# Optimization experiments

Measured on AMD Instinct MI355X. Metric: run time of the kernel, lower is better.

The kernel has to match this reference:

```python
import jax, jax.numpy as jnp
import numpy as np

B, S, DD, DE, DA = 32, 2048, 1024, 1024, 1024
NEG = -1000000000.0


def setup_inputs() -> dict:
    key = jax.random.key(0)
    k1, k2, k3, k4, k5 = jax.random.split(key, 5)
    query_state = jax.random.normal(k1, (B, DD), dtype=jnp.float32)
    encoder_hidden_states = jax.random.normal(k2, (B, S, DE), dtype=jnp.float32)
    attention_mask = jax.random.randint(k3, (B, S), 0, 2, dtype=jnp.int32)
    # W_c: Linear(DD+DE -> DA, bias=False): weight shape [DA, DD+DE]
    W_c = jax.random.normal(k4, (DA, DD + DE), dtype=jnp.float32) / np.sqrt(DD + DE)
    # V: Linear(DA -> 1, bias=False): weight shape [1, DA]
    V = jax.random.normal(k5, (1, DA), dtype=jnp.float32) / np.sqrt(DA)
    return {
        "query_state": query_state,
        "encoder_hidden_states": encoder_hidden_states,
        "attention_mask": attention_mask,
        "W_c": W_c,
        "V": V,
    }


def reference(query_state, encoder_hidden_states, attention_mask, W_c, V):
    # Split W_c along input dim: cat([q, e]) @ W_c.T == q @ Wq.T + e @ We.T
    Wq = W_c[:, :DD]          # [DA, DD]
    We = W_c[:, DD:]          # [DA, DE]
    q_proj = jnp.einsum('bd,ad->ba', query_state, Wq)            # [B, DA]
    e_proj = jnp.einsum('bsd,ad->bsa', encoder_hidden_states, We)  # [B, S, DA]
    energies = jnp.tanh(q_proj[:, None, :] + e_proj)             # [B, S, DA]
    scores = jnp.einsum('bsa,a->bs', energies, V[0])             # [B, S]
    scores = jnp.where(attention_mask == 0, NEG, scores)
    attention_weights = jax.nn.softmax(scores, axis=1)           # [B, S]
    context_vector = jnp.einsum('bs,bsd->bd', attention_weights, encoder_hidden_states)
    return context_vector, attention_weights
```

## Files before the change

kernel.cpp:

```cpp
#include <hip/hip_runtime.h>
#include <hip/hip_bf16.h>

#define NB 32
#define NS 2048
#define NDD 1024
#define NDE 1024
#define NDA 1024
#define NEGV (-1000000000.0f)

typedef __attribute__((ext_vector_type(8))) __bf16 bf16x8;
typedef __attribute__((ext_vector_type(4))) float f32x4;

__device__ __forceinline__ float fast_tanh(float x) {
    x = fminf(10.0f, fmaxf(-10.0f, x));
    float e = __expf(2.0f * x);
    return __fdividef(e - 1.0f, e + 1.0f);
}

__device__ __forceinline__ float bfu2f(unsigned short v) {
    union { unsigned u; float f; } c; c.u = (unsigned)v << 16; return c.f;
}

__global__ void prep_we(const float* __restrict__ Wc, __bf16* __restrict__ We) {
    int f = blockIdx.x * 256 + threadIdx.x;
    int a  = f >> 8;
    int k4 = f & 255;
    float4 v = *reinterpret_cast<const float4*>(Wc + (size_t)a * (NDD + NDE) + NDD + k4 * 4);
    union { __bf16 h[4]; uint2 u; } pk;
    pk.h[0] = (__bf16)v.x; pk.h[1] = (__bf16)v.y;
    pk.h[2] = (__bf16)v.z; pk.h[3] = (__bf16)v.w;
    *reinterpret_cast<uint2*>(We + (size_t)a * NDE + k4 * 4) = pk.u;
}

__global__ void prep_e(const float* __restrict__ E, __bf16* __restrict__ Eb) {
    size_t i = ((size_t)blockIdx.x * 256 + threadIdx.x) * 8;
    f32x4 x = __builtin_nontemporal_load(reinterpret_cast<const f32x4*>(E + i));
    f32x4 y = __builtin_nontemporal_load(reinterpret_cast<const f32x4*>(E + i + 4));
    union { __bf16 h[8]; uint4 u; } pk;
    pk.h[0] = (__bf16)x[0]; pk.h[1] = (__bf16)x[1]; pk.h[2] = (__bf16)x[2]; pk.h[3] = (__bf16)x[3];
    pk.h[4] = (__bf16)y[0]; pk.h[5] = (__bf16)y[1]; pk.h[6] = (__bf16)y[2]; pk.h[7] = (__bf16)y[3];
    *reinterpret_cast<uint4*>(Eb + i) = pk.u;
}

__global__ void qproj_kernel(const float* __restrict__ q, const float* __restrict__ Wc,
                             float* __restrict__ qp) {
    __shared__ float qs[NDD];
    int b = blockIdx.y;
    int a = blockIdx.x * 256 + threadIdx.x;
    float4 qv = *reinterpret_cast<const float4*>(q + (size_t)b * NDD + threadIdx.x * 4);
    *reinterpret_cast<float4*>(qs + threadIdx.x * 4) = qv;
    __syncthreads();
    const float* wrow = Wc + (size_t)a * (NDD + NDE);
    float acc = 0.f;
#pragma unroll 4
    for (int k4 = 0; k4 < 256; ++k4) {
        float4 w = *reinterpret_cast<const float4*>(wrow + k4 * 4);
        acc += qs[k4*4+0] * w.x + qs[k4*4+1] * w.y + qs[k4*4+2] * w.z + qs[k4*4+3] * w.w;
    }
    qp[(size_t)b * NDA + a] = acc;
}

__global__ __launch_bounds__(512, 2) void score256(
    const __bf16* __restrict__ Eb, const __bf16* __restrict__ We,
    const float* __restrict__ qp, const float* __restrict__ Vv,
    float* __restrict__ sp) {
    __shared__ __align__(16) __bf16 As[2][256 * 64];
    __shared__ __align__(16) __bf16 Bs[2][256 * 64];

    const int tid  = threadIdx.x;
    const int lane = tid & 63;
    const int l15  = lane & 15;
    const int h    = lane >> 4;
    const int wid  = tid >> 6;
    const int wr   = wid >> 2;
    const int wc   = wid & 3;

    const int bid = blockIdx.x;
    const int xcd = bid & 7;
    const int j   = bid >> 3;
    const int m   = xcd * 32 + (j >> 2);
    const int n   = j & 3;
    const int row0  = m * 256;
    const int ncol0 = n * 256;
    const int b     = m >> 3;

    f32x4 acc[8][4];
#pragma unroll
    for (int mf = 0; mf < 8; ++mf)
#pragma unroll
        for (int nf = 0; nf < 4; ++nf)
            acc[mf][nf] = (f32x4){0.f, 0.f, 0.f, 0.f};

    int offE[4], offW[4];
#pragma unroll
    for (int i = 0; i < 4; ++i) {
        int rr = i * 64 + (tid >> 3);
        int sg = (tid & 7) ^ (rr & 7);
        offE[i] = (row0  + rr) * 1024 + sg * 8;
        offW[i] = (ncol0 + rr) * 1024 + sg * 8;
    }

    const int slot0 = ((h ^ (l15 & 7)) * 16);
    const int aoffl = (wr * 128 + l15) * 128 + slot0;
    const int boffl = (wc * 64  + l15) * 128 + slot0;

#define STAGE8(abuf, bbuf, kc)                                                          \
    {                                                                                   \
        _Pragma("unroll")                                                               \
        for (int i = 0; i < 4; ++i)                                                     \
            __builtin_amdgcn_global_load_lds(                                           \
                (const __attribute__((address_space(1))) unsigned*)(Eb + offE[i] + (kc)),\
                (__attribute__((address_space(3))) unsigned*)((char*)(abuf) + i * 8192 + wid * 1024), \
                16, 0, 0);                                                              \
        _Pragma("unroll")                                                               \
        for (int i = 0; i < 4; ++i)                                                     \
            __builtin_amdgcn_global_load_lds(                                           \
                (const __attribute__((address_space(1))) unsigned*)(We + offW[i] + (kc)),\
                (__attribute__((address_space(3))) unsigned*)((char*)(bbuf) + i * 8192 + wid * 1024), \
                16, 0, 0);                                                              \
    }

    STAGE8(&As[0][0], &Bs[0][0], 0)
    float qv[4], vv[4];
#pragma unroll
    for (int nf = 0; nf < 4; ++nf) {
        int col = ncol0 + wc * 64 + nf * 16 + l15;
        qv[nf] = qp[(size_t)b * NDA + col];
        vv[nf] = Vv[col];
    }
    __syncthreads();

    for (int T = 0; T < 16; ++T) {
        const int cur = T & 1;
        const char* Ab = (const char*)&As[cur][0];
        const char* Bb = (const char*)&Bs[cur][0];
        if (T < 15) STAGE8(&As[cur ^ 1][0], &Bs[cur ^ 1][0], (T + 1) * 64)

        bf16x8 bfr[4][2], afr[4][2];
#pragma unroll
        for (int nf = 0; nf < 4; ++nf) {
            bfr[nf][0] = *reinterpret_cast<const bf16x8*>(Bb + (boffl + nf * 2048));
            bfr[nf][1] = *reinterpret_cast<const bf16x8*>(Bb + ((boffl + nf * 2048) ^ 64));
        }
#pragma unroll
        for (int mi = 0; mi < 4; ++mi) {
            afr[mi][0] = *reinterpret_cast<const bf16x8*>(Ab + (aoffl + mi * 2048));
            afr[mi][1] = *reinterpret_cast<const bf16x8*>(Ab + ((aoffl + mi * 2048) ^ 64));
        }
        __builtin_amdgcn_s_setprio(1);
#pragma unroll
        for (int ks = 0; ks < 2; ++ks)
#pragma unroll
            for (int mi = 0; mi < 4; ++mi)
#pragma unroll
                for (int nf = 0; nf < 4; ++nf)
                    acc[mi][nf] = __builtin_amdgcn_mfma_f32_16x16x32_bf16(afr[mi][ks], bfr[nf][ks], acc[mi][nf], 0, 0, 0);
        __builtin_amdgcn_s_setprio(0);
#pragma unroll
        for (int mi = 0; mi < 4; ++mi) {
            afr[mi][0] = *reinterpret_cast<const bf16x8*>(Ab + (aoffl + (4 + mi) * 2048));
            afr[mi][1] = *reinterpret_cast<const bf16x8*>(Ab + ((aoffl + (4 + mi) * 2048) ^ 64));
        }
        __builtin_amdgcn_s_setprio(1);
#pragma unroll
        for (int ks = 0; ks < 2; ++ks)
#pragma unroll
            for (int mi = 0; mi < 4; ++mi)
#pragma unroll
                for (int nf = 0; nf < 4; ++nf)
                    acc[4 + mi][nf] = __builtin_amdgcn_mfma_f32_16x16x32_bf16(afr[mi][ks], bfr[nf][ks], acc[4 + mi][nf], 0, 0, 0);
        __builtin_amdgcn_s_setprio(0);
        __syncthreads();
    }

    float* ps2 = reinterpret_cast<float*>(&As[0][0]);
#pragma unroll
    for (int mf = 0; mf < 8; ++mf)
#pragma unroll
        for (int jj = 0; jj < 4; ++jj) {
            float s = 0.f;
#pragma unroll
            for (int nf = 0; nf < 4; ++nf)
                s += fast_tanh(qv[nf] + acc[mf][nf][jj]) * vv[nf];
            s += __shfl_xor(s, 1);
            s += __shfl_xor(s, 2);
            s += __shfl_xor(s, 4);
            s += __shfl_xor(s, 8);
            if (l15 == 0)
                ps2[(wr * 128 + mf * 16 + h * 4 + jj) * 4 + wc] = s;
        }
    __syncthreads();
    if (tid < 256)
        sp[(size_t)n * (NB * NS) + row0 + tid] =
            ps2[tid * 4] + ps2[tid * 4 + 1] + ps2[tid * 4 + 2] + ps2[tid * 4 + 3];
}

__global__ void softmax_kernel(const float* __restrict__ sp, const int* __restrict__ mask,
                               float* __restrict__ wout, int np) {
    int b = blockIdx.x;
    const int* mrow = mask + (size_t)b * NS;
    float v[8];
    float lmax = -INFINITY;
#pragma unroll
    for (int jj = 0; jj < 8; ++jj) {
        int s = threadIdx.x + 256 * jj;
        float sc = 0.f;
        for (int nn = 0; nn < np; ++nn) sc += sp[(size_t)nn * (NB * NS) + b * NS + s];
        v[jj] = (mrow[s] == 0) ? NEGV : sc;
        lmax = fmaxf(lmax, v[jj]);
    }
#pragma unroll
    for (int mm = 1; mm <= 32; mm <<= 1) lmax = fmaxf(lmax, __shfl_xor(lmax, mm));
    __shared__ float redm[4], reds[4];
    if ((threadIdx.x & 63) == 0) redm[threadIdx.x >> 6] = lmax;
    __syncthreads();
    float bmax = fmaxf(fmaxf(redm[0], redm[1]), fmaxf(redm[2], redm[3]));
    float lsum = 0.f;
#pragma unroll
    for (int jj = 0; jj < 8; ++jj) { v[jj] = __expf(v[jj] - bmax); lsum += v[jj]; }
#pragma unroll
    for (int mm = 1; mm <= 32; mm <<= 1) lsum += __shfl_xor(lsum, mm);
    if ((threadIdx.x & 63) == 0) reds[threadIdx.x >> 6] = lsum;
    __syncthreads();
    float inv = __fdividef(1.0f, reds[0] + reds[1] + reds[2] + reds[3]);
#pragma unroll
    for (int jj = 0; jj < 8; ++jj) wout[(size_t)b * NS + threadIdx.x + 256 * jj] = v[jj] * inv;
}

__global__ void context_bf16(const __bf16* __restrict__ Eb, const float* __restrict__ w,
                             float* __restrict__ ctx) {
    int b  = blockIdx.x >> 3;
    int dc = blockIdx.x & 7;
    int dg = threadIdx.x & 31;
    int ss = threadIdx.x >> 5;
    const __bf16* base = Eb + (size_t)b * NS * NDE + (size_t)(ss * 256) * NDE + dc * 128 + dg * 4;
    const float* wb = w + (size_t)b * NS + ss * 256;
    float a0 = 0.f, a1 = 0.f, a2 = 0.f, a3 = 0.f;
#pragma unroll 8
    for (int s = 0; s < 256; ++s) {
        float ws = wb[s];
        uint2 u = *reinterpret_cast<const uint2*>(base + (size_t)s * NDE);
        a0 = fmaf(ws, bfu2f((unsigned short)(u.x & 0xffff)), a0);
        a1 = fmaf(ws, bfu2f((unsigned short)(u.x >> 16)), a1);
        a2 = fmaf(ws, bfu2f((unsigned short)(u.y & 0xffff)), a2);
        a3 = fmaf(ws, bfu2f((unsigned short)(u.y >> 16)), a3);
    }
    __shared__ float4 part[256];
    part[threadIdx.x] = make_float4(a0, a1, a2, a3);
    __syncthreads();
    if (threadIdx.x < 32) {
        float4 r = part[threadIdx.x];
#pragma unroll
        for (int k = 1; k < 8; ++k) {
            float4 p = part[threadIdx.x + 32 * k];
            r.x += p.x; r.y += p.y; r.z += p.z; r.w += p.w;
        }
        *reinterpret_cast<float4*>(ctx + (size_t)b * NDD + dc * 128 + threadIdx.x * 4) = r;
    }
}

extern "C" void kernel_launch(void* const* d_in, const int* in_sizes, int n_in,
                              void* d_out, int out_size, void* d_ws, size_t ws_size,
                              hipStream_t stream) {
    const float* query = (const float*)d_in[0];
    const float* enc   = (const float*)d_in[1];
    const int*   mask  = (const int*)d_in[2];
    const float* Wc    = (const float*)d_in[3];
    const float* V     = (const float*)d_in[4];

    float* out = (float*)d_out;
    float* ctx = out;
    float* wts = out + NB * NDD;

    const size_t WE_B = (size_t)NDA * NDE * 2;
    const size_t QP_B = (size_t)NB * NDA * 4;
    const size_t SP_B = (size_t)8 * NB * NS * 4;
    char* ws = (char*)d_ws;
    __bf16* We = (__bf16*)ws;
    float*  qp = (float*)(ws + WE_B);
    float*  sp = (float*)(ws + WE_B + QP_B);
    __bf16* Eb = (__bf16*)(ws + WE_B + QP_B + SP_B);

    hipLaunchKernelGGL(prep_we,      dim3(1024),  dim3(256), 0, stream, Wc, We);
    hipLaunchKernelGGL(qproj_kernel, dim3(4, NB), dim3(256), 0, stream, query, Wc, qp);
    hipLaunchKernelGGL(prep_e,       dim3(32768), dim3(256), 0, stream, enc, Eb);
    hipLaunchKernelGGL(score256,     dim3(1024),  dim3(512), 0, stream, Eb, We, qp, V, sp);
    hipLaunchKernelGGL(softmax_kernel, dim3(NB),  dim3(256), 0, stream, sp, mask, wts, 4);
    hipLaunchKernelGGL(context_bf16, dim3(256),   dim3(256), 0, stream, Eb, wts, ctx);
}
```

Before: 295.4 us.

## Split score GEMM tile across 16 waves with 1024-thread blocks

Doubles the score GEMM block from 512 to 1024 threads (16 waves in a 4x4 grid). Each wave now owns a 64x64 sub-tile instead of 128x64, halving per-wave accumulators and per-thread async loads per stage. The K loop is restructured to load and multiply one k-slice at a time. The aim is more waves to hide latency and lower register pressure. In exchange, occupancy falls to one block per CU, and each barrier now synchronizes more waves.

```diff
diff --git a/kernel.cpp b/kernel.cpp
--- a/kernel.cpp
+++ b/kernel.cpp
@@ -60,7 +60,7 @@
     qp[(size_t)b * NDA + a] = acc;
 }
 
-__global__ __launch_bounds__(512, 2) void score256(
+__global__ __launch_bounds__(1024, 1) void score256(
     const __bf16* __restrict__ Eb, const __bf16* __restrict__ We,
     const float* __restrict__ qp, const float* __restrict__ Vv,
     float* __restrict__ sp) {
@@ -84,43 +84,44 @@
     const int ncol0 = n * 256;
     const int b     = m >> 3;
 
-    f32x4 acc[8][4];
-#pragma unroll
-    for (int mf = 0; mf < 8; ++mf)
+    f32x4 acc[4][4];
+#pragma unroll
+    for (int mf = 0; mf < 4; ++mf)
 #pragma unroll
         for (int nf = 0; nf < 4; ++nf)
             acc[mf][nf] = (f32x4){0.f, 0.f, 0.f, 0.f};
 
-    int offE[4], offW[4];
-#pragma unroll
-    for (int i = 0; i < 4; ++i) {
-        int rr = i * 64 + (tid >> 3);
-        int sg = (tid & 7) ^ (rr & 7);
-        offE[i] = (row0  + rr) * 1024 + sg * 8;
-        offW[i] = (ncol0 + rr) * 1024 + sg * 8;
+    int offE[2], offW[2];
+#pragma unroll
+    for (int i = 0; i < 2; ++i) {
+        int chunk = i * 1024 + tid;
+        int r  = chunk >> 3;
+        int sg = (chunk & 7) ^ (r & 7);
+        offE[i] = (row0  + r) * 1024 + sg * 8;
+        offW[i] = (ncol0 + r) * 1024 + sg * 8;
     }
 
     const int slot0 = ((h ^ (l15 & 7)) * 16);
-    const int aoffl = (wr * 128 + l15) * 128 + slot0;
-    const int boffl = (wc * 64  + l15) * 128 + slot0;
-
-#define STAGE8(abuf, bbuf, kc)                                                          \
+    const int aoffl = (wr * 64 + l15) * 128 + slot0;
+    const int boffl = (wc * 64 + l15) * 128 + slot0;
+
+#define STAGE4(abuf, bbuf, kc)                                                          \
     {                                                                                   \
         _Pragma("unroll")                                                               \
-        for (int i = 0; i < 4; ++i)                                                     \
+        for (int i = 0; i < 2; ++i)                                                     \
             __builtin_amdgcn_global_load_lds(                                           \
                 (const __attribute__((address_space(1))) unsigned*)(Eb + offE[i] + (kc)),\
-                (__attribute__((address_space(3))) unsigned*)((char*)(abuf) + i * 8192 + wid * 1024), \
+                (__attribute__((address_space(3))) unsigned*)((char*)(abuf) + i * 16384 + wid * 1024), \
                 16, 0, 0);                                                              \
         _Pragma("unroll")                                                               \
-        for (int i = 0; i < 4; ++i)                                                     \
+        for (int i = 0; i < 2; ++i)                                                     \
             __builtin_amdgcn_global_load_lds(                                           \
                 (const __attribute__((address_space(1))) unsigned*)(We + offW[i] + (kc)),\
-                (__attribute__((address_space(3))) unsigned*)((char*)(bbuf) + i * 8192 + wid * 1024), \
+                (__attribute__((address_space(3))) unsigned*)((char*)(bbuf) + i * 16384 + wid * 1024), \
                 16, 0, 0);                                                              \
     }
 
-    STAGE8(&As[0][0], &Bs[0][0], 0)
+    STAGE4(&As[0][0], &Bs[0][0], 0)
     float qv[4], vv[4];
 #pragma unroll
     for (int nf = 0; nf < 4; ++nf) {
@@ -134,48 +135,31 @@
         const int cur = T & 1;
         const char* Ab = (const char*)&As[cur][0];
         const char* Bb = (const char*)&Bs[cur][0];
-        if (T < 15) STAGE8(&As[cur ^ 1][0], &Bs[cur ^ 1][0], (T + 1) * 64)
-
-        bf16x8 bfr[4][2], afr[4][2];
-#pragma unroll
-        for (int nf = 0; nf < 4; ++nf) {
-            bfr[nf][0] = *reinterpret_cast<const bf16x8*>(Bb + (boffl + nf * 2048));
-            bfr[nf][1] = *reinterpret_cast<const bf16x8*>(Bb + ((boffl + nf * 2048) ^ 64));
+        if (T < 15) STAGE4(&As[cur ^ 1][0], &Bs[cur ^ 1][0], (T + 1) * 64)
+
+#pragma unroll
+        for (int ks = 0; ks < 2; ++ks) {
+            bf16x8 bfr[4], afr[4];
+#pragma unroll
+            for (int nf = 0; nf < 4; ++nf)
+                bfr[nf] = *reinterpret_cast<const bf16x8*>(Bb + ((boffl + nf * 2048) ^ (ks * 64)));
+#pragma unroll
+            for (int mf = 0; mf < 4; ++mf)
+                afr[mf] = *reinterpret_cast<const bf16x8*>(Ab + ((aoffl + mf * 2048) ^ (ks * 64)));
+            __builtin_amdgcn_s_setprio(1);
+#pragma unroll
+            for (int mf = 0; mf < 4; ++mf)
+#pragma unroll
+                for (int nf = 0; nf < 4; ++nf)
+                    acc[mf][nf] = __builtin_amdgcn_mfma_f32_16x16x32_bf16(afr[mf], bfr[nf], acc[mf][nf], 0, 0, 0);
+            __builtin_amdgcn_s_setprio(0);
         }
-#pragma unroll
-        for (int mi = 0; mi < 4; ++mi) {
-            afr[mi][0] = *reinterpret_cast<const bf16x8*>(Ab + (aoffl + mi * 2048));
-            afr[mi][1] = *reinterpret_cast<const bf16x8*>(Ab + ((aoffl + mi * 2048) ^ 64));
-        }
-        __builtin_amdgcn_s_setprio(1);
-#pragma unroll
-        for (int ks = 0; ks < 2; ++ks)
-#pragma unroll
-            for (int mi = 0; mi < 4; ++mi)
-#pragma unroll
-                for (int nf = 0; nf < 4; ++nf)
-                    acc[mi][nf] = __builtin_amdgcn_mfma_f32_16x16x32_bf16(afr[mi][ks], bfr[nf][ks], acc[mi][nf], 0, 0, 0);
-        __builtin_amdgcn_s_setprio(0);
-#pragma unroll
-        for (int mi = 0; mi < 4; ++mi) {
-            afr[mi][0] = *reinterpret_cast<const bf16x8*>(Ab + (aoffl + (4 + mi) * 2048));
-            afr[mi][1] = *reinterpret_cast<const bf16x8*>(Ab + ((aoffl + (4 + mi) * 2048) ^ 64));
-        }
-        __builtin_amdgcn_s_setprio(1);
-#pragma unroll
-        for (int ks = 0; ks < 2; ++ks)
-#pragma unroll
-            for (int mi = 0; mi < 4; ++mi)
-#pragma unroll
-                for (int nf = 0; nf < 4; ++nf)
-                    acc[4 + mi][nf] = __builtin_amdgcn_mfma_f32_16x16x32_bf16(afr[mi][ks], bfr[nf][ks], acc[4 + mi][nf], 0, 0, 0);
-        __builtin_amdgcn_s_setprio(0);
         __syncthreads();
     }
 
     float* ps2 = reinterpret_cast<float*>(&As[0][0]);
 #pragma unroll
-    for (int mf = 0; mf < 8; ++mf)
+    for (int mf = 0; mf < 4; ++mf)
 #pragma unroll
         for (int jj = 0; jj < 4; ++jj) {
             float s = 0.f;
@@ -187,7 +171,7 @@
             s += __shfl_xor(s, 4);
             s += __shfl_xor(s, 8);
             if (l15 == 0)
-                ps2[(wr * 128 + mf * 16 + h * 4 + jj) * 4 + wc] = s;
+                ps2[(wr * 64 + mf * 16 + h * 4 + jj) * 4 + wc] = s;
         }
     __syncthreads();
     if (tid < 256)
@@ -284,7 +268,7 @@
     hipLaunchKernelGGL(prep_we,      dim3(1024),  dim3(256), 0, stream, Wc, We);
     hipLaunchKernelGGL(qproj_kernel, dim3(4, NB), dim3(256), 0, stream, query, Wc, qp);
     hipLaunchKernelGGL(prep_e,       dim3(32768), dim3(256), 0, stream, enc, Eb);
-    hipLaunchKernelGGL(score256,     dim3(1024),  dim3(512), 0, stream, Eb, We, qp, V, sp);
+    hipLaunchKernelGGL(score256,     dim3(1024),  dim3(1024), 0, stream, Eb, We, qp, V, sp);
     hipLaunchKernelGGL(softmax_kernel, dim3(NB),  dim3(256), 0, stream, sp, mask, wts, 4);
     hipLaunchKernelGGL(context_bf16, dim3(256),   dim3(256), 0, stream, Eb, wts, ctx);
 }
```

Measured after the change: 289.6 us (median of 2 runs). No clear change (-2.0%).
